# Kernel optimization log

Measured on AMD Instinct MI355X. Metric: run time of the kernel, lower is better.

Reference implementation:

```python
import jax, jax.numpy as jnp
import numpy as np

IN_FEATURES = 4096
IN_CHANNELS = 21
WINDOW = 32
STRIDES = 1
OUT_CHANNELS = 8
EPS = 1e-7
N_WIN = int((IN_FEATURES - WINDOW) / STRIDES - EPS) + 1  # 4064
NK = OUT_CHANNELS * N_WIN                                # 32512
D = IN_CHANNELS * WINDOW                                 # 672


def _window_starts():
    # windows 0..n_win-2 start at j*strides; last window anchored at in_features-window_size
    s = np.arange(N_WIN) * STRIDES
    s[-1] = IN_FEATURES - WINDOW
    return jnp.asarray(s, dtype=jnp.int32)


def setup_inputs() -> dict:
    key = jax.random.key(0)
    k1, k2 = jax.random.split(key)
    x = jax.random.normal(k1, (32, IN_CHANNELS, IN_FEATURES), dtype=jnp.float32)
    # matches torch init: 2*(rand-0.5)/sqrt(window_size*in_channels)
    weight = (jax.random.uniform(k2, (NK, D), dtype=jnp.float32) - 0.5) * 2.0 / np.sqrt(D)
    return {"x": x, "weight": weight}


def reference(x, weight):
    # x: (B, C, F); the sparse fbank matmul is an im2col gather of strided windows
    B = x.shape[0]
    starts = _window_starts()                        # (n_win,)
    idx = starts[:, None] + jnp.arange(WINDOW)       # (n_win, W)
    win = x[:, :, idx]                               # (B, C, n_win, W)
    # fbank row layout is channel-major (k, w) -> flatten as C*W
    win = jnp.transpose(win, (0, 2, 1, 3)).reshape(B, N_WIN, D)  # (B, n_win, C*W)
    # each window is replicated out_channels times in Nk; weight rows grouped per window
    w = weight.reshape(N_WIN, OUT_CHANNELS, D)
    out = jnp.einsum('bjd,jod->bjo', win, w)         # (B, n_win, out_channels)
    return out.reshape(B, NK)
```

## Files before the change

### kernel.cpp

```cpp
#include <hip/hip_runtime.h>
#include <hip/hip_bf16.h>


#define NF 4096
#define NC 21
#define WIN 32
#define OC 8
#define NWIN 4064
#define NKTOT (OC * NWIN)
#define DD (NC * WIN)
#define JB 8
#define NBLK (NWIN / JB)
#define XROWB 272
#define XBUFB 9216

typedef short short8 __attribute__((ext_vector_type(8)));
typedef float f32x4 __attribute__((ext_vector_type(4)));

static __device__ __forceinline__ short f2bf(float f) {
  __bf16 h = (__bf16)f;
  return __builtin_bit_cast(short, h);
}
static __device__ __forceinline__ short8 pk8(float a, float b, float c, float d,
                                             float e, float f, float g, float h) {
  short8 v;
  v[0]=f2bf(a); v[1]=f2bf(b); v[2]=f2bf(c); v[3]=f2bf(d);
  v[4]=f2bf(e); v[5]=f2bf(f); v[6]=f2bf(g); v[7]=f2bf(h);
  return v;
}
static __device__ __forceinline__ short8 sel8(f32x4 a, f32x4 b, f32x4 c, int u) {
  switch (u & 3) {
    case 0:  return pk8(a[0],a[1],a[2],a[3],b[0],b[1],b[2],b[3]);
    case 1:  return pk8(a[1],a[2],a[3],b[0],b[1],b[2],b[3],c[0]);
    case 2:  return pk8(a[2],a[3],b[0],b[1],b[2],b[3],c[0],c[1]);
    default: return pk8(a[3],b[0],b[1],b[2],b[3],c[0],c[1],c[2]);
  }
}

#define STAGE(GP, I, NB) \
  __builtin_amdgcn_global_load_lds( \
    (const __attribute__((address_space(1))) unsigned int*)(GP), \
    (__attribute__((address_space(3))) unsigned int*)(xlds + (NB)*XBUFB + (I)*1024), \
    16, 0, 0)

__global__ __launch_bounds__(256) void fb_stage(const float* __restrict__ x,
                                                const float* __restrict__ w,
                                                float* __restrict__ out) {
  __shared__ __align__(16) char xlds[2 * XBUFB];
  const int lane = threadIdx.x & 63;
  const int wv   = threadIdx.x >> 6;

  const int orig = blockIdx.x;
  const int xcd = orig & 7, idx = orig >> 3;
  const int blk = (xcd < 4 ? xcd * 64 : 256 + (xcd - 4) * 63) + idx;
  const int j0 = blk * JB;
  const int a0 = (j0 < NF - 68) ? j0 : (NF - 68);

  const int n  = lane & 15;
  const int o  = n & 7;
  const int Ck = (lane >> 4) * 2;
  const int boff0 = n * XROWB, boff1 = (16 + n) * XROWB;

  const int jg0 = j0 + 2 * wv, jg1 = jg0 + 1;
  const int s1v = (jg1 == NWIN - 1) ? (NF - WIN) : jg1;
  const int rj0 = jg0 - a0, rj1 = s1v - a0;
  const int u0 = rj0 & 3, u1 = rj1 & 3;
  const int Cw0 = rj0 >> 2, Cw1 = rj1 >> 2;

  const int i0 = 2 * wv, i1 = 2 * wv + 1;
  int q0 = i0 * 64 + lane, q1 = i1 * 64 + lane, q2 = 512 + lane;
  if (q2 > 543) q2 = 543;
  const int b0 = q0 / 17, p0 = q0 - b0 * 17;
  const int b1 = q1 / 17, p1 = q1 - b1 * 17;
  const int b2 = q2 / 17, p2 = q2 - b2 * 17;
  const float* xs0 = x + (size_t)b0 * (NC * NF) + a0 + p0 * 4;
  const float* xs1 = x + (size_t)b1 * (NC * NF) + a0 + p1 * 4;
  const float* xs2 = x + (size_t)b2 * (NC * NF) + a0 + p2 * 4;

  const float* wn0 = w + ((size_t)jg0 * OC + o) * DD + Ck * 4;
  const float* wn1 = w + ((size_t)jg1 * OC + o) * DD + Ck * 4;

  f32x4 acc00 = {0,0,0,0}, acc01 = {0,0,0,0}, acc10 = {0,0,0,0}, acc11 = {0,0,0,0};

  STAGE(xs0, i0, 0); xs0 += NF;
  STAGE(xs1, i1, 0); xs1 += NF;
  if (wv == 0) { STAGE(xs2, 8, 0); xs2 += NF; }
  float4 w0a = *(const float4*)(wn0), w0b = *(const float4*)(wn0 + 4);
  float4 w1a = *(const float4*)(wn1), w1b = *(const float4*)(wn1 + 4);
  wn0 += WIN; wn1 += WIN;
  __syncthreads();

  int buf = 0;
  for (int c = 0; c < NC; ++c) {
    float4 w0an = {0,0,0,0}, w0bn = {0,0,0,0}, w1an = {0,0,0,0}, w1bn = {0,0,0,0};
    if (c < NC - 1) {
      STAGE(xs0, i0, buf ^ 1); xs0 += NF;
      STAGE(xs1, i1, buf ^ 1); xs1 += NF;
      if (wv == 0) { STAGE(xs2, 8, buf ^ 1); xs2 += NF; }
      w0an = *(const float4*)(wn0); w0bn = *(const float4*)(wn0 + 4);
      w1an = *(const float4*)(wn1); w1bn = *(const float4*)(wn1 + 4);
      wn0 += WIN; wn1 += WIN;
    }
    const char* xb = xlds + buf * XBUFB;
    {
      short8 fbw = pk8(w0a.x,w0a.y,w0a.z,w0a.w,w0b.x,w0b.y,w0b.z,w0b.w);
      int off = boff0 + (Cw0 + Ck) * 16;
      f32x4 ra = *(const f32x4*)(xb + off);
      f32x4 rb = *(const f32x4*)(xb + off + 16);
      f32x4 rc = *(const f32x4*)(xb + off + 32);
      acc00 = __builtin_amdgcn_mfma_f32_16x16x32_bf16(sel8(ra,rb,rc,u0), fbw, acc00, 0,0,0);
      off = boff1 + (Cw0 + Ck) * 16;
      ra = *(const f32x4*)(xb + off);
      rb = *(const f32x4*)(xb + off + 16);
      rc = *(const f32x4*)(xb + off + 32);
      acc01 = __builtin_amdgcn_mfma_f32_16x16x32_bf16(sel8(ra,rb,rc,u0), fbw, acc01, 0,0,0);
    }
    {
      short8 fbw = pk8(w1a.x,w1a.y,w1a.z,w1a.w,w1b.x,w1b.y,w1b.z,w1b.w);
      int off = boff0 + (Cw1 + Ck) * 16;
      f32x4 ra = *(const f32x4*)(xb + off);
      f32x4 rb = *(const f32x4*)(xb + off + 16);
      f32x4 rc = *(const f32x4*)(xb + off + 32);
      acc10 = __builtin_amdgcn_mfma_f32_16x16x32_bf16(sel8(ra,rb,rc,u1), fbw, acc10, 0,0,0);
      off = boff1 + (Cw1 + Ck) * 16;
      ra = *(const f32x4*)(xb + off);
      rb = *(const f32x4*)(xb + off + 16);
      rc = *(const f32x4*)(xb + off + 32);
      acc11 = __builtin_amdgcn_mfma_f32_16x16x32_bf16(sel8(ra,rb,rc,u1), fbw, acc11, 0,0,0);
    }
    __syncthreads();
    w0a = w0an; w0b = w0bn; w1a = w1an; w1b = w1bn;
    buf ^= 1;
  }

  if (n < 8) {
    const int m0 = (lane >> 4) * 4;
    #pragma unroll
    for (int e = 0; e < 4; ++e) {
      out[(size_t)(m0 + e)      * NKTOT + (size_t)jg0 * OC + n] = acc00[e];
      out[(size_t)(m0 + e + 16) * NKTOT + (size_t)jg0 * OC + n] = acc01[e];
      out[(size_t)(m0 + e)      * NKTOT + (size_t)jg1 * OC + n] = acc10[e];
      out[(size_t)(m0 + e + 16) * NKTOT + (size_t)jg1 * OC + n] = acc11[e];
    }
  }
}

extern "C" void kernel_launch(void* const* d_in, const int* in_sizes, int n_in,
                              void* d_out, int out_size, void* d_ws, size_t ws_size,
                              hipStream_t stream) {
  const float* x = (const float*)d_in[0];
  const float* w = (const float*)d_in[1];
  float* out = (float*)d_out;
  dim3 grid(NBLK), block(256);
  hipLaunchKernelGGL(fb_stage, grid, block, 0, stream, x, w, out);
}
```

Baseline: 29.38 us.

## Triple-buffer LDS staging with explicit vmcnt waits and single barrier per step

Replaces the double-buffered LDS pipeline with a three-buffer ring that prefetches the input two channels ahead. The two __syncthreads per iteration become one s_waitcnt vmcnt with a hand-chosen count plus one s_barrier, and the loop is fully unrolled. The aim is to hide global-to-LDS latency and cut synchronisation stalls. The hand-coded vmcnt counts depend on the exact number of outstanding loads per wave, including the weight loads, so a miscount could cause races. LDS use also grows by half.

```diff
diff --git a/kernel.cpp b/kernel.cpp
--- a/kernel.cpp
+++ b/kernel.cpp
@@ -37,16 +37,24 @@
   }
 }
 
+static __device__ __forceinline__ void wait_vmcnt(int n) {
+  switch (n) {
+    case 4: asm volatile("s_waitcnt vmcnt(4)" ::: "memory"); break;
+    case 6: asm volatile("s_waitcnt vmcnt(6)" ::: "memory"); break;
+    default: asm volatile("s_waitcnt vmcnt(7)" ::: "memory"); break;
+  }
+}
+
 #define STAGE(GP, I, NB) \
   __builtin_amdgcn_global_load_lds( \
     (const __attribute__((address_space(1))) unsigned int*)(GP), \
     (__attribute__((address_space(3))) unsigned int*)(xlds + (NB)*XBUFB + (I)*1024), \
     16, 0, 0)
 
-__global__ __launch_bounds__(256) void fb_stage(const float* __restrict__ x,
-                                                const float* __restrict__ w,
-                                                float* __restrict__ out) {
-  __shared__ __align__(16) char xlds[2 * XBUFB];
+__global__ __launch_bounds__(256) void fb_pipe(const float* __restrict__ x,
+                                               const float* __restrict__ w,
+                                               float* __restrict__ out) {
+  __shared__ __align__(16) char xlds[3 * XBUFB];
   const int lane = threadIdx.x & 63;
   const int wv   = threadIdx.x >> 6;
 
@@ -82,26 +90,37 @@
 
   f32x4 acc00 = {0,0,0,0}, acc01 = {0,0,0,0}, acc10 = {0,0,0,0}, acc11 = {0,0,0,0};
 
-  STAGE(xs0, i0, 0); xs0 += NF;
-  STAGE(xs1, i1, 0); xs1 += NF;
-  if (wv == 0) { STAGE(xs2, 8, 0); xs2 += NF; }
+  STAGE(xs0, i0, 0); STAGE(xs1, i1, 0);
+  if (wv == 0) { STAGE(xs2, 8, 0); }
+  xs0 += NF; xs1 += NF; xs2 += NF;
+  STAGE(xs0, i0, 1); STAGE(xs1, i1, 1);
+  if (wv == 0) { STAGE(xs2, 8, 1); }
+  xs0 += NF; xs1 += NF; xs2 += NF;
   float4 w0a = *(const float4*)(wn0), w0b = *(const float4*)(wn0 + 4);
   float4 w1a = *(const float4*)(wn1), w1b = *(const float4*)(wn1 + 4);
   wn0 += WIN; wn1 += WIN;
-  __syncthreads();
 
-  int buf = 0;
+  #pragma unroll
   for (int c = 0; c < NC; ++c) {
+    if (c < NC - 1) wait_vmcnt(wv == 0 ? 7 : 6);
+    else            wait_vmcnt(4);
+    __builtin_amdgcn_s_barrier();
+    __builtin_amdgcn_sched_barrier(0);
+
+    if (c + 2 < NC) {
+      const int nb = (c + 2) % 3;
+      STAGE(xs0, i0, nb); STAGE(xs1, i1, nb);
+      if (wv == 0) { STAGE(xs2, 8, nb); }
+      xs0 += NF; xs1 += NF; xs2 += NF;
+    }
     float4 w0an = {0,0,0,0}, w0bn = {0,0,0,0}, w1an = {0,0,0,0}, w1bn = {0,0,0,0};
-    if (c < NC - 1) {
-      STAGE(xs0, i0, buf ^ 1); xs0 += NF;
-      STAGE(xs1, i1, buf ^ 1); xs1 += NF;
-      if (wv == 0) { STAGE(xs2, 8, buf ^ 1); xs2 += NF; }
+    if (c + 1 < NC) {
       w0an = *(const float4*)(wn0); w0bn = *(const float4*)(wn0 + 4);
       w1an = *(const float4*)(wn1); w1bn = *(const float4*)(wn1 + 4);
       wn0 += WIN; wn1 += WIN;
     }
-    const char* xb = xlds + buf * XBUFB;
+
+    const char* xb = xlds + (c % 3) * XBUFB;
     {
       short8 fbw = pk8(w0a.x,w0a.y,w0a.z,w0a.w,w0b.x,w0b.y,w0b.z,w0b.w);
       int off = boff0 + (Cw0 + Ck) * 16;
@@ -128,9 +147,7 @@
       rc = *(const f32x4*)(xb + off + 32);
       acc11 = __builtin_amdgcn_mfma_f32_16x16x32_bf16(sel8(ra,rb,rc,u1), fbw, acc11, 0,0,0);
     }
-    __syncthreads();
     w0a = w0an; w0b = w0bn; w1a = w1an; w1b = w1bn;
-    buf ^= 1;
   }
 
   if (n < 8) {
@@ -152,5 +169,5 @@
   const float* w = (const float*)d_in[1];
   float* out = (float*)d_out;
   dim3 grid(NBLK), block(256);
-  hipLaunchKernelGGL(fb_stage, grid, block, 0, stream, x, w, out);
+  hipLaunchKernelGGL(fb_pipe, grid, block, 0, stream, x, w, out);
 }
```

Measured after the change: 29.48 us. Within noise of the previous version (+0.4%).

## Deepen pipeline to triple-buffered LDS with manual vmcnt waits and full unroll

Applied to the files above, without the earlier changes.

Replaces the double-buffered channel loop with a fully unrolled 21-step schedule that uses three LDS buffers for x (prefetch two channels ahead) and four register sets for weights (three channels ahead). __syncthreads is replaced by explicit s_waitcnt vmcnt counts plus a raw s_barrier, so outstanding global loads are not drained every iteration. The intent is to hide global-load latency better. It costs more LDS and registers, and correctness now depends on hand-counted vmcnt values that must match the compiler's load ordering.

```diff
diff --git a/kernel.cpp b/kernel.cpp
--- a/kernel.cpp
+++ b/kernel.cpp
@@ -37,16 +37,18 @@
   }
 }
 
-#define STAGE(GP, I, NB) \
+#define VMW(N) asm volatile("s_waitcnt vmcnt(" #N ")" ::: "memory")
+#define BAR() { __builtin_amdgcn_s_barrier(); __builtin_amdgcn_sched_barrier(0); }
+
+#define GLL(GP, LOFF) \
   __builtin_amdgcn_global_load_lds( \
     (const __attribute__((address_space(1))) unsigned int*)(GP), \
-    (__attribute__((address_space(3))) unsigned int*)(xlds + (NB)*XBUFB + (I)*1024), \
-    16, 0, 0)
+    (__attribute__((address_space(3))) unsigned int*)(xlds + (LOFF)), 16, 0, 0)
 
-__global__ __launch_bounds__(256) void fb_stage(const float* __restrict__ x,
-                                                const float* __restrict__ w,
-                                                float* __restrict__ out) {
-  __shared__ __align__(16) char xlds[2 * XBUFB];
+__global__ __launch_bounds__(256) void fb_deep(const float* __restrict__ x,
+                                               const float* __restrict__ w,
+                                               float* __restrict__ out) {
+  __shared__ __align__(16) char xlds[3 * XBUFB];
   const int lane = threadIdx.x & 63;
   const int wv   = threadIdx.x >> 6;
 
@@ -76,62 +78,91 @@
   const float* xs0 = x + (size_t)b0 * (NC * NF) + a0 + p0 * 4;
   const float* xs1 = x + (size_t)b1 * (NC * NF) + a0 + p1 * 4;
   const float* xs2 = x + (size_t)b2 * (NC * NF) + a0 + p2 * 4;
+  const int l0 = i0 * 1024, l1 = i1 * 1024, l2 = 8 * 1024;
 
-  const float* wn0 = w + ((size_t)jg0 * OC + o) * DD + Ck * 4;
-  const float* wn1 = w + ((size_t)jg1 * OC + o) * DD + Ck * 4;
+  const float* wb0 = w + ((size_t)jg0 * OC + o) * DD + Ck * 4;
+  const float* wb1 = w + ((size_t)jg1 * OC + o) * DD + Ck * 4;
 
   f32x4 acc00 = {0,0,0,0}, acc01 = {0,0,0,0}, acc10 = {0,0,0,0}, acc11 = {0,0,0,0};
 
-  STAGE(xs0, i0, 0); xs0 += NF;
-  STAGE(xs1, i1, 0); xs1 += NF;
-  if (wv == 0) { STAGE(xs2, 8, 0); xs2 += NF; }
-  float4 w0a = *(const float4*)(wn0), w0b = *(const float4*)(wn0 + 4);
-  float4 w1a = *(const float4*)(wn1), w1b = *(const float4*)(wn1 + 4);
-  wn0 += WIN; wn1 += WIN;
-  __syncthreads();
+  f32x4 wA0a, wA0b, wA1a, wA1b, wB0a, wB0b, wB1a, wB1b;
+  f32x4 wC0a, wC0b, wC1a, wC1b, wD0a, wD0b, wD1a, wD1b;
 
-  int buf = 0;
-  for (int c = 0; c < NC; ++c) {
-    float4 w0an = {0,0,0,0}, w0bn = {0,0,0,0}, w1an = {0,0,0,0}, w1bn = {0,0,0,0};
-    if (c < NC - 1) {
-      STAGE(xs0, i0, buf ^ 1); xs0 += NF;
-      STAGE(xs1, i1, buf ^ 1); xs1 += NF;
-      if (wv == 0) { STAGE(xs2, 8, buf ^ 1); xs2 += NF; }
-      w0an = *(const float4*)(wn0); w0bn = *(const float4*)(wn0 + 4);
-      w1an = *(const float4*)(wn1); w1bn = *(const float4*)(wn1 + 4);
-      wn0 += WIN; wn1 += WIN;
-    }
-    const char* xb = xlds + buf * XBUFB;
-    {
-      short8 fbw = pk8(w0a.x,w0a.y,w0a.z,w0a.w,w0b.x,w0b.y,w0b.z,w0b.w);
-      int off = boff0 + (Cw0 + Ck) * 16;
-      f32x4 ra = *(const f32x4*)(xb + off);
-      f32x4 rb = *(const f32x4*)(xb + off + 16);
-      f32x4 rc = *(const f32x4*)(xb + off + 32);
-      acc00 = __builtin_amdgcn_mfma_f32_16x16x32_bf16(sel8(ra,rb,rc,u0), fbw, acc00, 0,0,0);
-      off = boff1 + (Cw0 + Ck) * 16;
-      ra = *(const f32x4*)(xb + off);
-      rb = *(const f32x4*)(xb + off + 16);
-      rc = *(const f32x4*)(xb + off + 32);
-      acc01 = __builtin_amdgcn_mfma_f32_16x16x32_bf16(sel8(ra,rb,rc,u0), fbw, acc01, 0,0,0);
-    }
-    {
-      short8 fbw = pk8(w1a.x,w1a.y,w1a.z,w1a.w,w1b.x,w1b.y,w1b.z,w1b.w);
-      int off = boff0 + (Cw1 + Ck) * 16;
-      f32x4 ra = *(const f32x4*)(xb + off);
-      f32x4 rb = *(const f32x4*)(xb + off + 16);
-      f32x4 rc = *(const f32x4*)(xb + off + 32);
-      acc10 = __builtin_amdgcn_mfma_f32_16x16x32_bf16(sel8(ra,rb,rc,u1), fbw, acc10, 0,0,0);
-      off = boff1 + (Cw1 + Ck) * 16;
-      ra = *(const f32x4*)(xb + off);
-      rb = *(const f32x4*)(xb + off + 16);
-      rc = *(const f32x4*)(xb + off + 32);
-      acc11 = __builtin_amdgcn_mfma_f32_16x16x32_bf16(sel8(ra,rb,rc,u1), fbw, acc11, 0,0,0);
-    }
-    __syncthreads();
-    w0a = w0an; w0b = w0bn; w1a = w1an; w1b = w1bn;
-    buf ^= 1;
-  }
+#define STG(CH, NB) { \
+    GLL(xs0 + (CH) * NF, (NB) * XBUFB + l0); \
+    GLL(xs1 + (CH) * NF, (NB) * XBUFB + l1); \
+    if (wv == 0) { GLL(xs2 + (CH) * NF, (NB) * XBUFB + l2); } }
+
+#define LOADW(CH, P) { \
+    w##P##0a = *(const f32x4*)(wb0 + (CH) * WIN); \
+    w##P##0b = *(const f32x4*)(wb0 + (CH) * WIN + 4); \
+    w##P##1a = *(const f32x4*)(wb1 + (CH) * WIN); \
+    w##P##1b = *(const f32x4*)(wb1 + (CH) * WIN + 4); }
+
+#define COMPUTE(C, P) { \
+    const char* xb_ = xlds + ((C) % 3) * XBUFB; \
+    { short8 fbw = pk8(w##P##0a[0],w##P##0a[1],w##P##0a[2],w##P##0a[3], \
+                       w##P##0b[0],w##P##0b[1],w##P##0b[2],w##P##0b[3]); \
+      int off = boff0 + (Cw0 + Ck) * 16; \
+      f32x4 ra = *(const f32x4*)(xb_ + off); \
+      f32x4 rb = *(const f32x4*)(xb_ + off + 16); \
+      f32x4 rc = *(const f32x4*)(xb_ + off + 32); \
+      acc00 = __builtin_amdgcn_mfma_f32_16x16x32_bf16(sel8(ra,rb,rc,u0), fbw, acc00, 0,0,0); \
+      off = boff1 + (Cw0 + Ck) * 16; \
+      ra = *(const f32x4*)(xb_ + off); \
+      rb = *(const f32x4*)(xb_ + off + 16); \
+      rc = *(const f32x4*)(xb_ + off + 32); \
+      acc01 = __builtin_amdgcn_mfma_f32_16x16x32_bf16(sel8(ra,rb,rc,u0), fbw, acc01, 0,0,0); } \
+    { short8 fbw = pk8(w##P##1a[0],w##P##1a[1],w##P##1a[2],w##P##1a[3], \
+                       w##P##1b[0],w##P##1b[1],w##P##1b[2],w##P##1b[3]); \
+      int off = boff0 + (Cw1 + Ck) * 16; \
+      f32x4 ra = *(const f32x4*)(xb_ + off); \
+      f32x4 rb = *(const f32x4*)(xb_ + off + 16); \
+      f32x4 rc = *(const f32x4*)(xb_ + off + 32); \
+      acc10 = __builtin_amdgcn_mfma_f32_16x16x32_bf16(sel8(ra,rb,rc,u1), fbw, acc10, 0,0,0); \
+      off = boff1 + (Cw1 + Ck) * 16; \
+      ra = *(const f32x4*)(xb_ + off); \
+      rb = *(const f32x4*)(xb_ + off + 16); \
+      rc = *(const f32x4*)(xb_ + off + 32); \
+      acc11 = __builtin_amdgcn_mfma_f32_16x16x32_bf16(sel8(ra,rb,rc,u1), fbw, acc11, 0,0,0); } }
+
+#define BODY(C, CUR, DST) { \
+    if ((C) + 2 <= 20) { STG((C) + 2, ((C) + 2) % 3); } \
+    if ((C) + 3 <= 20) { LOADW((C) + 3, DST); } \
+    COMPUTE(C, CUR); }
+
+#define WMID() { if (wv == 0) { VMW(11); } else { VMW(10); } }
+#define W19()  { if (wv == 0) { VMW(7);  } else { VMW(6);  } }
+
+  STG(0, 0); STG(1, 1);
+  LOADW(0, A); LOADW(1, B); LOADW(2, C);
+
+  VMW(8);  BAR(); BODY(0,  A, D);
+  WMID();  BAR(); BODY(1,  B, A);
+  WMID();  BAR(); BODY(2,  C, B);
+  WMID();  BAR(); BODY(3,  D, C);
+  WMID();  BAR(); BODY(4,  A, D);
+  WMID();  BAR(); BODY(5,  B, A);
+  WMID();  BAR(); BODY(6,  C, B);
+  WMID();  BAR(); BODY(7,  D, C);
+  WMID();  BAR(); BODY(8,  A, D);
+  WMID();  BAR(); BODY(9,  B, A);
+  WMID();  BAR(); BODY(10, C, B);
+  WMID();  BAR(); BODY(11, D, C);
+  WMID();  BAR(); BODY(12, A, D);
+  WMID();  BAR(); BODY(13, B, A);
+  WMID();  BAR(); BODY(14, C, B);
+  WMID();  BAR(); BODY(15, D, C);
+  WMID();  BAR(); BODY(16, A, D);
+  WMID();  BAR(); BODY(17, B, A);
+  WMID();  BAR(); BODY(18, C, B);
+  W19();   BAR(); BODY(19, D, C);
+  VMW(0);  BAR(); BODY(20, A, D);
+
+#undef BODY
+#undef COMPUTE
+#undef LOADW
+#undef STG
 
   if (n < 8) {
     const int m0 = (lane >> 4) * 4;
@@ -152,5 +183,5 @@
   const float* w = (const float*)d_in[1];
   float* out = (float*)d_out;
   dim3 grid(NBLK), block(256);
-  hipLaunchKernelGGL(fb_stage, grid, block, 0, stream, x, w, out);
+  hipLaunchKernelGGL(fb_deep, grid, block, 0, stream, x, w, out);
 }
```

Result: slower. 31.37 us (+6.8%).

## Use 16-window blocks with 8 waves and triple-buffered LDS staging pipeline

Applied to the files above, without the earlier changes.

Doubles the windows per block to 16 with 512 threads, so each staged x tile is shared by more waves and the redundant halo loads per window drop. The LDS staging moves from double to triple buffering with an explicit vmcnt wait and a single barrier per channel, which lets loads run two channels ahead. The per-channel weight loads are fully unrolled with constant offsets. In exchange the grid halves to 254 blocks, lowering block-level parallelism on a large GPU, and the hand-written vmcnt counts must match the issued loads exactly to stay correct.

```diff
diff --git a/kernel.cpp b/kernel.cpp
--- a/kernel.cpp
+++ b/kernel.cpp
@@ -9,10 +9,11 @@
 #define NWIN 4064
 #define NKTOT (OC * NWIN)
 #define DD (NC * WIN)
-#define JB 8
+#define JB 16
 #define NBLK (NWIN / JB)
-#define XROWB 272
-#define XBUFB 9216
+#define CHK 13
+#define XROWB (CHK * 16)
+#define XBUFB (32 * XROWB)
 
 typedef short short8 __attribute__((ext_vector_type(8)));
 typedef float f32x4 __attribute__((ext_vector_type(4)));
@@ -37,104 +38,106 @@
   }
 }
 
-#define STAGE(GP, I, NB) \
+#define VMW(N) asm volatile("s_waitcnt vmcnt(" #N ")" ::: "memory")
+#define BAR() { __builtin_amdgcn_s_barrier(); __builtin_amdgcn_sched_barrier(0); }
+
+#define GLL(GP, LOFF) \
   __builtin_amdgcn_global_load_lds( \
     (const __attribute__((address_space(1))) unsigned int*)(GP), \
-    (__attribute__((address_space(3))) unsigned int*)(xlds + (NB)*XBUFB + (I)*1024), \
-    16, 0, 0)
+    (__attribute__((address_space(3))) unsigned int*)(xlds + (LOFF)), 16, 0, 0)
 
-__global__ __launch_bounds__(256) void fb_stage(const float* __restrict__ x,
-                                                const float* __restrict__ w,
-                                                float* __restrict__ out) {
-  __shared__ __align__(16) char xlds[2 * XBUFB];
-  const int lane = threadIdx.x & 63;
-  const int wv   = threadIdx.x >> 6;
+__global__ __launch_bounds__(512) void fb_j16(const float* __restrict__ x,
+                                              const float* __restrict__ w,
+                                              float* __restrict__ out) {
+  __shared__ __align__(16) char xlds[3 * XBUFB + 1024];
+  const int tid  = threadIdx.x;
+  const int lane = tid & 63;
+  const int wv   = tid >> 6;
 
   const int orig = blockIdx.x;
   const int xcd = orig & 7, idx = orig >> 3;
-  const int blk = (xcd < 4 ? xcd * 64 : 256 + (xcd - 4) * 63) + idx;
+  const int blk = (xcd < 6 ? xcd * 32 : 192 + (xcd - 6) * 31) + idx;
   const int j0 = blk * JB;
-  const int a0 = (j0 < NF - 68) ? j0 : (NF - 68);
 
   const int n  = lane & 15;
   const int o  = n & 7;
-  const int Ck = (lane >> 4) * 2;
+  const int hi = lane >> 4;
+  const int Ckb = hi * 32;
   const int boff0 = n * XROWB, boff1 = (16 + n) * XROWB;
 
   const int jg0 = j0 + 2 * wv, jg1 = jg0 + 1;
-  const int s1v = (jg1 == NWIN - 1) ? (NF - WIN) : jg1;
-  const int rj0 = jg0 - a0, rj1 = s1v - a0;
+  const int s1  = (jg1 == NWIN - 1) ? (NF - WIN) : jg1;
+  const int rj0 = 2 * wv, rj1 = s1 - j0;
   const int u0 = rj0 & 3, u1 = rj1 & 3;
-  const int Cw0 = rj0 >> 2, Cw1 = rj1 >> 2;
+  const int o00 = boff0 + (rj0 >> 2) * 16 + Ckb;
+  const int o01 = boff1 + (rj0 >> 2) * 16 + Ckb;
+  const int o10 = boff0 + (rj1 >> 2) * 16 + Ckb;
+  const int o11 = boff1 + (rj1 >> 2) * 16 + Ckb;
 
-  const int i0 = 2 * wv, i1 = 2 * wv + 1;
-  int q0 = i0 * 64 + lane, q1 = i1 * 64 + lane, q2 = 512 + lane;
-  if (q2 > 543) q2 = 543;
-  const int b0 = q0 / 17, p0 = q0 - b0 * 17;
-  const int b1 = q1 / 17, p1 = q1 - b1 * 17;
-  const int b2 = q2 / 17, p2 = q2 - b2 * 17;
-  const float* xs0 = x + (size_t)b0 * (NC * NF) + a0 + p0 * 4;
-  const float* xs1 = x + (size_t)b1 * (NC * NF) + a0 + p1 * 4;
-  const float* xs2 = x + (size_t)b2 * (NC * NF) + a0 + p2 * 4;
+  int q = (tid <= 415) ? tid : 415;
+  const int row = q / CHK, cs = q - row * CHK;
+  const int csc = (cs <= 11) ? cs : 11;
+  const float* xsp = x + (size_t)row * (NC * NF) + j0 + csc * 4;
+  const int sdo = wv * 1024;
 
-  const float* wn0 = w + ((size_t)jg0 * OC + o) * DD + Ck * 4;
-  const float* wn1 = w + ((size_t)jg1 * OC + o) * DD + Ck * 4;
+#define STG(CH, NB) { \
+    if (wv < 6)       { GLL(xsp + (CH) * NF, (NB) * XBUFB + sdo); } \
+    else if (wv == 6) { if (lane < 32) { GLL(xsp + (CH) * NF, (NB) * XBUFB + sdo); } } }
+
+  const float* wp0 = w + ((size_t)jg0 * OC + o) * DD + hi * 8;
+  const float* wp1 = w + ((size_t)jg1 * OC + o) * DD + hi * 8;
 
   f32x4 acc00 = {0,0,0,0}, acc01 = {0,0,0,0}, acc10 = {0,0,0,0}, acc11 = {0,0,0,0};
 
-  STAGE(xs0, i0, 0); xs0 += NF;
-  STAGE(xs1, i1, 0); xs1 += NF;
-  if (wv == 0) { STAGE(xs2, 8, 0); xs2 += NF; }
-  float4 w0a = *(const float4*)(wn0), w0b = *(const float4*)(wn0 + 4);
-  float4 w1a = *(const float4*)(wn1), w1b = *(const float4*)(wn1 + 4);
-  wn0 += WIN; wn1 += WIN;
-  __syncthreads();
+  STG(0, 0);
+  STG(1, 1);
+  float4 w0a = *(const float4*)(wp0), w0b = *(const float4*)(wp0 + 4);
+  float4 w1a = *(const float4*)(wp1), w1b = *(const float4*)(wp1 + 4);
 
-  int buf = 0;
+  #pragma unroll
   for (int c = 0; c < NC; ++c) {
+    if (c < NC - 1) { VMW(5); } else { VMW(0); }
+    BAR();
+
+    if (c + 2 < NC) { STG(c + 2, (c + 2) % 3); }
     float4 w0an = {0,0,0,0}, w0bn = {0,0,0,0}, w1an = {0,0,0,0}, w1bn = {0,0,0,0};
-    if (c < NC - 1) {
-      STAGE(xs0, i0, buf ^ 1); xs0 += NF;
-      STAGE(xs1, i1, buf ^ 1); xs1 += NF;
-      if (wv == 0) { STAGE(xs2, 8, buf ^ 1); xs2 += NF; }
-      w0an = *(const float4*)(wn0); w0bn = *(const float4*)(wn0 + 4);
-      w1an = *(const float4*)(wn1); w1bn = *(const float4*)(wn1 + 4);
-      wn0 += WIN; wn1 += WIN;
+    if (c + 1 < NC) {
+      w0an = *(const float4*)(wp0 + (c + 1) * WIN);
+      w0bn = *(const float4*)(wp0 + (c + 1) * WIN + 4);
+      w1an = *(const float4*)(wp1 + (c + 1) * WIN);
+      w1bn = *(const float4*)(wp1 + (c + 1) * WIN + 4);
     }
-    const char* xb = xlds + buf * XBUFB;
+
+    const char* xb = xlds + (c % 3) * XBUFB;
     {
       short8 fbw = pk8(w0a.x,w0a.y,w0a.z,w0a.w,w0b.x,w0b.y,w0b.z,w0b.w);
-      int off = boff0 + (Cw0 + Ck) * 16;
-      f32x4 ra = *(const f32x4*)(xb + off);
-      f32x4 rb = *(const f32x4*)(xb + off + 16);
-      f32x4 rc = *(const f32x4*)(xb + off + 32);
+      f32x4 ra = *(const f32x4*)(xb + o00);
+      f32x4 rb = *(const f32x4*)(xb + o00 + 16);
+      f32x4 rc = *(const f32x4*)(xb + o00 + 32);
       acc00 = __builtin_amdgcn_mfma_f32_16x16x32_bf16(sel8(ra,rb,rc,u0), fbw, acc00, 0,0,0);
-      off = boff1 + (Cw0 + Ck) * 16;
-      ra = *(const f32x4*)(xb + off);
-      rb = *(const f32x4*)(xb + off + 16);
-      rc = *(const f32x4*)(xb + off + 32);
+      ra = *(const f32x4*)(xb + o01);
+      rb = *(const f32x4*)(xb + o01 + 16);
+      rc = *(const f32x4*)(xb + o01 + 32);
       acc01 = __builtin_amdgcn_mfma_f32_16x16x32_bf16(sel8(ra,rb,rc,u0), fbw, acc01, 0,0,0);
     }
     {
       short8 fbw = pk8(w1a.x,w1a.y,w1a.z,w1a.w,w1b.x,w1b.y,w1b.z,w1b.w);
-      int off = boff0 + (Cw1 + Ck) * 16;
-      f32x4 ra = *(const f32x4*)(xb + off);
-      f32x4 rb = *(const f32x4*)(xb + off + 16);
-      f32x4 rc = *(const f32x4*)(xb + off + 32);
+      f32x4 ra = *(const f32x4*)(xb + o10);
+      f32x4 rb = *(const f32x4*)(xb + o10 + 16);
+      f32x4 rc = *(const f32x4*)(xb + o10 + 32);
       acc10 = __builtin_amdgcn_mfma_f32_16x16x32_bf16(sel8(ra,rb,rc,u1), fbw, acc10, 0,0,0);
-      off = boff1 + (Cw1 + Ck) * 16;
-      ra = *(const f32x4*)(xb + off);
-      rb = *(const f32x4*)(xb + off + 16);
-      rc = *(const f32x4*)(xb + off + 32);
+      ra = *(const f32x4*)(xb + o11);
+      rb = *(const f32x4*)(xb + o11 + 16);
+      rc = *(const f32x4*)(xb + o11 + 32);
       acc11 = __builtin_amdgcn_mfma_f32_16x16x32_bf16(sel8(ra,rb,rc,u1), fbw, acc11, 0,0,0);
     }
-    __syncthreads();
     w0a = w0an; w0b = w0bn; w1a = w1an; w1b = w1bn;
-    buf ^= 1;
   }
 
+#undef STG
+
   if (n < 8) {
-    const int m0 = (lane >> 4) * 4;
+    const int m0 = hi * 4;
     #pragma unroll
     for (int e = 0; e < 4; ++e) {
       out[(size_t)(m0 + e)      * NKTOT + (size_t)jg0 * OC + n] = acc00[e];
@@ -151,6 +154,6 @@
   const float* x = (const float*)d_in[0];
   const float* w = (const float*)d_in[1];
   float* out = (float*)d_out;
-  dim3 grid(NBLK), block(256);
-  hipLaunchKernelGGL(fb_stage, grid, block, 0, stream, x, w, out);
+  dim3 grid(NBLK), block(512);
+  hipLaunchKernelGGL(fb_j16, grid, block, 0, stream, x, w, out);
 }
```

Result: slower. 33.41 us (+13.7%).
